# Kernel optimization log

Hardware: AMD Instinct MI355X
Metric: run time of the kernel (lower is better)

Reference implementation:

```python
import jax, jax.numpy as jnp
import numpy as np

HID = 768
POS = 768
TGT = 20
LBL = 30522
EPS = 1e-5


def layer_norm(x, g, b):
    mu = jnp.mean(x, axis=-1, keepdims=True)
    var = jnp.mean((x - mu) ** 2, axis=-1, keepdims=True)
    return (x - mu) * jax.lax.rsqrt(var + EPS) * g + b


def setup_inputs() -> dict:
    key = jax.random.key(0)
    ks = jax.random.split(key, 12)
    bs, n_node, num_pairs = 4, 512, 128
    inp = {
        "input_nodes": jax.random.normal(ks[0], (bs, n_node, HID), dtype=jnp.float32),
        "pairs": jax.random.randint(ks[1], (bs, num_pairs, 2), 0, n_node - 1, dtype=jnp.int64),
        "pos_emb": jax.random.normal(ks[2], (TGT, POS), dtype=jnp.float32) * 0.02,
        "W1": jax.random.normal(ks[3], (2 * HID + POS, HID), dtype=jnp.float32) * 0.02,
        "b1": jnp.zeros((HID,), dtype=jnp.float32),
        "g1": jnp.ones((HID,), dtype=jnp.float32),
        "be1": jnp.zeros((HID,), dtype=jnp.float32),
        "W2": jax.random.normal(ks[4], (HID, HID), dtype=jnp.float32) * 0.02,
        "b2": jnp.zeros((HID,), dtype=jnp.float32),
        "g2": jnp.ones((HID,), dtype=jnp.float32),
        "be2": jnp.zeros((HID,), dtype=jnp.float32),
        "Wd": jax.random.normal(ks[5], (HID, LBL), dtype=jnp.float32) * 0.02,
        "bd": jnp.zeros((LBL,), dtype=jnp.float32),
    }
    return inp


def reference(input_nodes, pairs, pos_emb, W1, b1, g1, be1, W2, b2, g2, be2, Wd, bd):
    bs, num_pairs, _ = pairs.shape
    dim = input_nodes.shape[-1]
    left = pairs[:, :, 0] + 1   # [bs, np]
    right = pairs[:, :, 1] + 1
    # gather paired node features: [bs, np, dim]
    lh = jnp.take_along_axis(input_nodes, left[:, :, None], axis=1)
    rh = jnp.take_along_axis(input_nodes, right[:, :, None], axis=1)
    R = bs * num_pairs
    lh = jnp.broadcast_to(lh.reshape(R, 1, dim), (R, TGT, dim))
    rh = jnp.broadcast_to(rh.reshape(R, 1, dim), (R, TGT, dim))
    pe = jnp.broadcast_to(pos_emb[None, :, :], (R, TGT, POS))
    x = jnp.concatenate((lh, rh, pe), axis=-1)  # [R, TGT, 2*HID+POS]
    h = layer_norm(jax.nn.gelu(x @ W1 + b1), g1, be1)
    h = layer_norm(jax.nn.gelu(h @ W2 + b2), g2, be2)
    return h @ Wd + bd  # [R, TGT, LBL]
```

## Files before the change

### kernel.cpp

```cpp
#include <hip/hip_runtime.h>
#include <stdint.h>
#include <math.h>

typedef unsigned short u16;
typedef unsigned int u32;

#define HID   768
#define TGT   20
#define LBL   30522
#define RPAIR 512
#define ROWS  10240
#define KCAT  1536
#define NPAD2 30720

typedef float  f32x4  __attribute__((ext_vector_type(4)));
typedef __bf16 bf16x8 __attribute__((ext_vector_type(8)));

__device__ __forceinline__ u16 f2bf(float f) {
  u32 u = __float_as_uint(f);
  u += 0x7fffu + ((u >> 16) & 1u);
  return (u16)(u >> 16);
}
__device__ __forceinline__ float bf2f(u16 h) {
  return __uint_as_float(((u32)h) << 16);
}
__device__ __forceinline__ float gelu_tanh(float x) {
  float x3 = x * x * x;
  float t = tanhf(0.7978845608028654f * (x + 0.044715f * x3));
  return 0.5f * x * (1.0f + t);
}

__device__ __forceinline__ void async16(u16* lds, const u16* g) {
  __builtin_amdgcn_global_load_lds(
      (__attribute__((address_space(1))) void*)const_cast<u16*>(g),
      (__attribute__((address_space(3))) void*)lds,
      16, 0, 0);
}

#define BARRIER() do { asm volatile("" ::: "memory"); __builtin_amdgcn_s_barrier(); asm volatile("" ::: "memory"); } while (0)

__global__ __launch_bounds__(256) void tconv_kernel(const float* __restrict__ B,
                                                    u16* __restrict__ Bt,
                                                    int K, int N, int Npad) {
  __shared__ u16 tile[32][34];
  int n0 = blockIdx.x * 32, k0 = blockIdx.y * 32;
  int tx = threadIdx.x & 31, ty = threadIdx.x >> 5;
#pragma unroll
  for (int i = 0; i < 4; i++) {
    int kk = ty + i * 8;
    int k = k0 + kk, n = n0 + tx;
    float v = (k < K && n < N) ? B[(size_t)k * N + n] : 0.0f;
    tile[kk][tx] = f2bf(v);
  }
  __syncthreads();
#pragma unroll
  for (int i = 0; i < 4; i++) {
    int nn = ty + i * 8;
    int n = n0 + nn, k = k0 + tx;
    if (n < Npad && k < K) Bt[(size_t)n * K + k] = tile[tx][nn];
  }
}

__global__ __launch_bounds__(256) void gather_kernel(const float* __restrict__ nodes,
                                                     const int* __restrict__ p32,
                                                     u16* __restrict__ A1) {
  int idx = blockIdx.x * 256 + threadIdx.x;
  if (idx >= RPAIR * KCAT) return;
  bool is64 = ((p32[1] | p32[3] | p32[5] | p32[7] | p32[9] | p32[11] | p32[13] | p32[15]) == 0);
  int r = idx / KCAT, c = idx - r * KCAT;
  int b = r >> 7, p = r & 127;
  int which = (c >= HID) ? 1 : 0;
  int cc = which ? (c - HID) : c;
  int slot = (b * 128 + p) * 2 + which;
  int node = (is64 ? p32[slot * 2] : p32[slot]) + 1;
  float v = nodes[((size_t)(b * 512 + node)) * HID + cc];
  A1[idx] = f2bf(v);
}

__global__ __launch_bounds__(256) void peproj_kernel(const float* __restrict__ pos_emb,
                                                     const float* __restrict__ W1,
                                                     const float* __restrict__ b1,
                                                     float* __restrict__ pep) {
  __shared__ float pe[HID];
  int t = blockIdx.x, tid = threadIdx.x;
  for (int i = tid; i < HID; i += 256) pe[i] = pos_emb[t * HID + i];
  __syncthreads();
  float acc0 = 0.f, acc1 = 0.f, acc2 = 0.f;
  const float* Wp = W1 + (size_t)KCAT * HID;
  for (int k = 0; k < HID; k++) {
    float p = pe[k];
    const float* wr = Wp + (size_t)k * HID;
    acc0 = fmaf(p, wr[tid], acc0);
    acc1 = fmaf(p, wr[tid + 256], acc1);
    acc2 = fmaf(p, wr[tid + 512], acc2);
  }
  pep[t * HID + tid]       = acc0 + b1[tid];
  pep[t * HID + tid + 256] = acc1 + b1[tid + 256];
  pep[t * HID + tid + 512] = acc2 + b1[tid + 512];
}

template <int EPI>
__global__ __launch_bounds__(256) void gemm_bt(const u16* __restrict__ A,
                                               const u16* __restrict__ Bt,
                                               const float* __restrict__ bias,
                                               float* __restrict__ Cf,
                                               u16* __restrict__ Cb,
                                               int N, int K) {
  __shared__ __align__(16) u16 As[128 * 32];
  __shared__ __align__(16) u16 Bs[128 * 32];
  const int tid  = threadIdx.x;
  const int lane = tid & 63;
  const int w    = tid >> 6;
  const int wr   = w >> 1, wc = w & 1;
  const int m0 = blockIdx.y * 128;
  const int n0 = blockIdx.x * 128;

  f32x4 acc[4][4];
  const f32x4 fzero = {0.f, 0.f, 0.f, 0.f};
#pragma unroll
  for (int m = 0; m < 4; m++)
#pragma unroll
    for (int n = 0; n < 4; n++) acc[m][n] = fzero;

  const int srow = lane >> 2;
  const int scol = (lane & 3) * 8;
  const int nkt = K >> 5;

  for (int kt = 0; kt < nkt; ++kt) {
    const int k0 = kt << 5;
#pragma unroll
    for (int j = 0; j < 2; j++) {
      int rbase = w * 32 + j * 16;
      async16(&As[rbase * 32], A + (size_t)(m0 + rbase + srow) * K + k0 + scol);
      async16(&Bs[rbase * 32], Bt + (size_t)(n0 + rbase + srow) * K + k0 + scol);
    }
    asm volatile("s_waitcnt vmcnt(0)" ::: "memory");
    __syncthreads();

    bf16x8 a[4], b[4];
    const int kk = (lane >> 4) * 8;
#pragma unroll
    for (int m = 0; m < 4; m++)
      a[m] = *reinterpret_cast<const bf16x8*>(&As[(wr * 64 + m * 16 + (lane & 15)) * 32 + kk]);
#pragma unroll
    for (int n = 0; n < 4; n++)
      b[n] = *reinterpret_cast<const bf16x8*>(&Bs[(wc * 64 + n * 16 + (lane & 15)) * 32 + kk]);
#pragma unroll
    for (int m = 0; m < 4; m++)
#pragma unroll
      for (int n = 0; n < 4; n++)
        acc[m][n] = __builtin_amdgcn_mfma_f32_16x16x32_bf16(a[m], b[n], acc[m][n], 0, 0, 0);
    __syncthreads();
  }

  const int rr = (lane >> 4) * 4;
  const int cc = lane & 15;
#pragma unroll
  for (int m = 0; m < 4; m++) {
#pragma unroll
    for (int n = 0; n < 4; n++) {
      int col = n0 + wc * 64 + n * 16 + cc;
#pragma unroll
      for (int j = 0; j < 4; j++) {
        int row = m0 + wr * 64 + m * 16 + rr + j;
        float v = acc[m][n][j];
        if (EPI == 0) {
          Cf[(size_t)row * N + col] = v;
        } else {
          v = gelu_tanh(v + bias[col]);
          Cb[(size_t)row * N + col] = f2bf(v);
        }
      }
    }
  }
}

__global__ __launch_bounds__(512, 2) void gemm256_head(const u16* __restrict__ A,
                                                       const u16* __restrict__ B,
                                                       const float* __restrict__ bias,
                                                       float* __restrict__ C) {
  __shared__ __align__(16) u16 As[2][256 * 64];
  __shared__ __align__(16) u16 Bs[2][256 * 64];
  const int tid  = threadIdx.x;
  const int lane = tid & 63;
  const int wid  = tid >> 6;
  const int wm   = wid >> 2;
  const int wn   = wid & 3;

  int orig = blockIdx.x;
  int l = (orig & 7) * 600 + (orig >> 3);
  int mt = l / 120, nt = l - mt * 120;
  const int m0 = mt * 256, n0 = nt * 256;
  const int nkt = 12;

  f32x4 acc[8][4];
  const f32x4 fzero = {0.f, 0.f, 0.f, 0.f};
#pragma unroll
  for (int mi = 0; mi < 8; mi++)
#pragma unroll
    for (int ni = 0; ni < 4; ni++) acc[mi][ni] = fzero;

  const int sl_r = lane >> 3;
  const int sl_c = ((lane & 7) ^ sl_r) * 8;
  auto stage_half = [&](const u16* src, int grow0, u16* ldsReg, int half, int ke0) {
#pragma unroll
    for (int j = 0; j < 2; j++) {
      int rowb = half * 128 + (j * 8 + wid) * 8;
      const u16* gp = src + (size_t)(grow0 + rowb + sl_r) * 768 + ke0 + sl_c;
      async16(ldsReg + rowb * 64, gp);
    }
  };
  auto lda = [&](const u16* buf, int mi, int ks) -> bf16x8 {
    int row = wm * 128 + mi * 16 + (lane & 15);
    int kch = ks * 4 + (lane >> 4);
    return *reinterpret_cast<const bf16x8*>(&buf[row * 64 + ((kch ^ (row & 7)) << 3)]);
  };
  auto ldb = [&](const u16* buf, int ni, int ks) -> bf16x8 {
    int row = wn * 64 + ni * 16 + (lane & 15);
    int kch = ks * 4 + (lane >> 4);
    return *reinterpret_cast<const bf16x8*>(&buf[row * 64 + ((kch ^ (row & 7)) << 3)]);
  };

  stage_half(A, m0, As[0], 0, 0);
  stage_half(A, m0, As[0], 1, 0);
  stage_half(B, n0, Bs[0], 0, 0);
  stage_half(B, n0, Bs[0], 1, 0);
  stage_half(A, m0, As[1], 0, 64);
  stage_half(A, m0, As[1], 1, 64);
  asm volatile("s_waitcnt vmcnt(4)" ::: "memory");
  __builtin_amdgcn_sched_barrier(0);
  __builtin_amdgcn_s_barrier();
  asm volatile("" ::: "memory");

  bf16x8 aF[8][2];
  bf16x8 bF[4][2];

#define MFMA_QUAD(MI0, NI0)                                                        \
  do {                                                                             \
    __builtin_amdgcn_s_setprio(1);                                                 \
    _Pragma("unroll") for (int mi = (MI0); mi < (MI0) + 4; ++mi)                   \
      _Pragma("unroll") for (int ni = (NI0); ni < (NI0) + 2; ++ni)                 \
        _Pragma("unroll") for (int ks = 0; ks < 2; ++ks)                           \
          acc[mi][ni] = __builtin_amdgcn_mfma_f32_16x16x32_bf16(aF[mi][ks], bF[ni][ks], acc[mi][ni], 0, 0, 0); \
    __builtin_amdgcn_s_setprio(0);                                                 \
  } while (0)

#define WAIT_LGKM() do { asm volatile("s_waitcnt lgkmcnt(0)" ::: "memory"); __builtin_amdgcn_sched_barrier(0); } while (0)

  for (int t = 0; t < nkt; ++t) {
    const u16* Ab = As[t & 1];
    const u16* Bb = Bs[t & 1];
    u16* Bnext = Bs[(t + 1) & 1];
    u16* Acur  = As[t & 1];
    const int ke1 = (t + 1) * 64, ke2 = (t + 2) * 64;
    const bool sB = (t + 1) < nkt, sA = (t + 2) < nkt;

#pragma unroll
    for (int mi = 0; mi < 4; ++mi)
#pragma unroll
      for (int ks = 0; ks < 2; ++ks) aF[mi][ks] = lda(Ab, mi, ks);
#pragma unroll
    for (int ni = 0; ni < 2; ++ni)
#pragma unroll
      for (int ks = 0; ks < 2; ++ks) bF[ni][ks] = ldb(Bb, ni, ks);
    if (sB) stage_half(B, n0, Bnext, 0, ke1);
    BARRIER();
    WAIT_LGKM();
    MFMA_QUAD(0, 0);
    BARRIER();

#pragma unroll
    for (int mi = 4; mi < 8; ++mi)
#pragma unroll
      for (int ks = 0; ks < 2; ++ks) aF[mi][ks] = lda(Ab, mi, ks);
    if (sB) stage_half(B, n0, Bnext, 1, ke1);
    BARRIER();
    WAIT_LGKM();
    MFMA_QUAD(4, 0);
    BARRIER();

#pragma unroll
    for (int ni = 2; ni < 4; ++ni)
#pragma unroll
      for (int ks = 0; ks < 2; ++ks) bF[ni][ks] = ldb(Bb, ni, ks);
    if (sA) stage_half(A, m0, Acur, 0, ke2);
    BARRIER();
    WAIT_LGKM();
    MFMA_QUAD(4, 2);
    BARRIER();

    if (sA) stage_half(A, m0, Acur, 1, ke2);
    BARRIER();
    MFMA_QUAD(0, 2);
    if (t + 2 < nkt) {
      asm volatile("s_waitcnt vmcnt(4)" ::: "memory");
    } else if (t + 1 < nkt) {
      asm volatile("s_waitcnt vmcnt(0)" ::: "memory");
    }
    __builtin_amdgcn_sched_barrier(0);
    BARRIER();
  }
#undef MFMA_QUAD
#undef WAIT_LGKM

  const int r0 = m0 + wm * 128;
  const int c0 = n0 + wn * 64;
  const int rr = (lane >> 4) * 4;
  const int ccl = lane & 15;
#pragma unroll
  for (int ni = 0; ni < 4; ++ni) {
    int col = c0 + ni * 16 + ccl;
    if (col < LBL) {
      float bv = bias[col];
#pragma unroll
      for (int mi = 0; mi < 8; ++mi)
#pragma unroll
        for (int j = 0; j < 4; ++j) {
          int row = r0 + mi * 16 + rr + j;
          C[(size_t)row * LBL + col] = acc[mi][ni][j] + bv;
        }
    }
  }
}

__global__ __launch_bounds__(256) void fuse1_kernel(const float* __restrict__ s,
                                                    const float* __restrict__ pep,
                                                    const float* __restrict__ g1,
                                                    const float* __restrict__ be1,
                                                    u16* __restrict__ h1) {
  __shared__ float red[8];
  int g = blockIdx.x, tid = threadIdx.x;
  int r = g / TGT, t = g - r * TGT;
  const float* sr = s + (size_t)r * HID;
  const float* pt = pep + (size_t)t * HID;
  float y[3], s1 = 0.f, s2 = 0.f;
#pragma unroll
  for (int i = 0; i < 3; i++) {
    int j = tid + i * 256;
    float x = sr[j] + pt[j];
    y[i] = gelu_tanh(x);
    s1 += y[i];
    s2 += y[i] * y[i];
  }
#pragma unroll
  for (int off = 32; off > 0; off >>= 1) {
    s1 += __shfl_down(s1, off);
    s2 += __shfl_down(s2, off);
  }
  if ((tid & 63) == 0) { red[tid >> 6] = s1; red[4 + (tid >> 6)] = s2; }
  __syncthreads();
  float mean = (red[0] + red[1] + red[2] + red[3]) * (1.0f / HID);
  float var  = (red[4] + red[5] + red[6] + red[7]) * (1.0f / HID) - mean * mean;
  float inv  = rsqrtf(var + 1e-5f);
#pragma unroll
  for (int i = 0; i < 3; i++) {
    int j = tid + i * 256;
    h1[(size_t)g * HID + j] = f2bf((y[i] - mean) * inv * g1[j] + be1[j]);
  }
}

__global__ __launch_bounds__(256) void fuse2_kernel(const u16* __restrict__ G,
                                                    const float* __restrict__ g2,
                                                    const float* __restrict__ be2,
                                                    u16* __restrict__ h2) {
  __shared__ float red[8];
  int g = blockIdx.x, tid = threadIdx.x;
  const u16* gr = G + (size_t)g * HID;
  float y[3], s1 = 0.f, s2 = 0.f;
#pragma unroll
  for (int i = 0; i < 3; i++) {
    int j = tid + i * 256;
    y[i] = bf2f(gr[j]);
    s1 += y[i];
    s2 += y[i] * y[i];
  }
#pragma unroll
  for (int off = 32; off > 0; off >>= 1) {
    s1 += __shfl_down(s1, off);
    s2 += __shfl_down(s2, off);
  }
  if ((tid & 63) == 0) { red[tid >> 6] = s1; red[4 + (tid >> 6)] = s2; }
  __syncthreads();
  float mean = (red[0] + red[1] + red[2] + red[3]) * (1.0f / HID);
  float var  = (red[4] + red[5] + red[6] + red[7]) * (1.0f / HID) - mean * mean;
  float inv  = rsqrtf(var + 1e-5f);
#pragma unroll
  for (int i = 0; i < 3; i++) {
    int j = tid + i * 256;
    h2[(size_t)g * HID + j] = f2bf((y[i] - mean) * inv * g2[j] + be2[j]);
  }
}

extern "C" void kernel_launch(void* const* d_in, const int* in_sizes, int n_in,
                              void* d_out, int out_size, void* d_ws, size_t ws_size,
                              hipStream_t stream) {
  const float* input_nodes = (const float*)d_in[0];
  const int*   pairs       = (const int*)d_in[1];
  const float* pos_emb     = (const float*)d_in[2];
  const float* W1  = (const float*)d_in[3];
  const float* b1  = (const float*)d_in[4];
  const float* g1  = (const float*)d_in[5];
  const float* be1 = (const float*)d_in[6];
  const float* W2  = (const float*)d_in[7];
  const float* b2  = (const float*)d_in[8];
  const float* g2  = (const float*)d_in[9];
  const float* be2 = (const float*)d_in[10];
  const float* Wd  = (const float*)d_in[11];
  const float* bd  = (const float*)d_in[12];
  float* out = (float*)d_out;

  char* ws = (char*)d_ws;
  u16*   WdT   = (u16*)(ws + 0);
  u16*   W2T   = (u16*)(ws + 47185920);
  u16*   W1lrT = (u16*)(ws + 48365568);
  u16*   A1    = (u16*)(ws + 50724864);
  float* pep   = (float*)(ws + 52297728);
  float* sbuf  = (float*)(ws + 52359168);
  u16*   h1    = (u16*)(ws + 53932032);
  u16*   G     = (u16*)(ws + 69660672);

  tconv_kernel<<<dim3(960, 24), 256, 0, stream>>>(Wd, WdT, HID, LBL, NPAD2);
  tconv_kernel<<<dim3(24, 24), 256, 0, stream>>>(W2, W2T, HID, HID, HID);
  tconv_kernel<<<dim3(24, 48), 256, 0, stream>>>(W1, W1lrT, KCAT, HID, HID);
  gather_kernel<<<dim3((RPAIR * KCAT + 255) / 256), 256, 0, stream>>>(input_nodes, pairs, A1);
  peproj_kernel<<<dim3(TGT), 256, 0, stream>>>(pos_emb, W1, b1, pep);

  gemm_bt<0><<<dim3(6, 4), 256, 0, stream>>>(A1, W1lrT, nullptr, sbuf, nullptr, HID, KCAT);
  fuse1_kernel<<<dim3(ROWS), 256, 0, stream>>>(sbuf, pep, g1, be1, h1);

  gemm_bt<1><<<dim3(6, 80), 256, 0, stream>>>(h1, W2T, b2, nullptr, G, HID, HID);
  fuse2_kernel<<<dim3(ROWS), 256, 0, stream>>>(G, g2, be2, G);

  gemm256_head<<<dim3(4800), 512, 0, stream>>>(G, WdT, bd, out);
}
```

Measured before the change: 1.296 ms.

## Make head GEMM persistent, streaming tiles continuously across k-loop boundaries

```diff
diff --git a/kernel.cpp b/kernel.cpp
--- a/kernel.cpp
+++ b/kernel.cpp
@@ -38,6 +38,8 @@
 }
 
 #define BARRIER() do { asm volatile("" ::: "memory"); __builtin_amdgcn_s_barrier(); asm volatile("" ::: "memory"); } while (0)
+#define VMWAIT8() do { asm volatile("s_waitcnt vmcnt(8)" ::: "memory"); __builtin_amdgcn_sched_barrier(0); } while (0)
+#define VMWAIT0() do { asm volatile("s_waitcnt vmcnt(0)" ::: "memory"); __builtin_amdgcn_sched_barrier(0); } while (0)
 
 __global__ __launch_bounds__(256) void tconv_kernel(const float* __restrict__ B,
                                                     u16* __restrict__ Bt,
@@ -175,10 +177,10 @@
   }
 }
 
-__global__ __launch_bounds__(512, 2) void gemm256_head(const u16* __restrict__ A,
-                                                       const u16* __restrict__ B,
-                                                       const float* __restrict__ bias,
-                                                       float* __restrict__ C) {
+__global__ __launch_bounds__(512, 2) void gemm256_stream(const u16* __restrict__ A,
+                                                         const u16* __restrict__ B,
+                                                         const float* __restrict__ bias,
+                                                         float* __restrict__ C) {
   __shared__ __align__(16) u16 As[2][256 * 64];
   __shared__ __align__(16) u16 Bs[2][256 * 64];
   const int tid  = threadIdx.x;
@@ -187,11 +189,11 @@
   const int wm   = wid >> 2;
   const int wn   = wid & 3;
 
-  int orig = blockIdx.x;
-  int l = (orig & 7) * 600 + (orig >> 3);
-  int mt = l / 120, nt = l - mt * 120;
-  const int m0 = mt * 256, n0 = nt * 256;
-  const int nkt = 12;
+  const int x  = blockIdx.x & 7;
+  const int jb = blockIdx.x >> 3;
+  const int t0 = (600 * jb) >> 5;
+  const int t1 = (600 * (jb + 1)) >> 5;
+  const int Q  = (t1 - t0) * 12;
 
   f32x4 acc[8][4];
   const f32x4 fzero = {0.f, 0.f, 0.f, 0.f};
@@ -202,12 +204,22 @@
 
   const int sl_r = lane >> 3;
   const int sl_c = ((lane & 7) ^ sl_r) * 8;
-  auto stage_half = [&](const u16* src, int grow0, u16* ldsReg, int half, int ke0) {
-#pragma unroll
-    for (int j = 0; j < 2; j++) {
-      int rowb = half * 128 + (j * 8 + wid) * 8;
-      const u16* gp = src + (size_t)(grow0 + rowb + sl_r) * 768 + ke0 + sl_c;
-      async16(ldsReg + rowb * 64, gp);
+
+  auto stage = [&](int q) {
+    int tt = t0 + q / 12;
+    int kt = q - (q / 12) * 12;
+    int mt = 5 * x + tt / 120;
+    int nt = tt - (tt / 120) * 120;
+    const int k0 = kt * 64;
+    u16* Ab = As[q & 1];
+    u16* Bb = Bs[q & 1];
+    const u16* Ag = A + (size_t)(mt * 256) * 768 + k0;
+    const u16* Bg = B + (size_t)(nt * 256) * 768 + k0;
+#pragma unroll
+    for (int jj = 0; jj < 4; jj++) {
+      int rbase = wid * 32 + jj * 8;
+      async16(Ab + rbase * 64, Ag + (size_t)(rbase + sl_r) * 768 + sl_c);
+      async16(Bb + rbase * 64, Bg + (size_t)(rbase + sl_r) * 768 + sl_c);
     }
   };
   auto lda = [&](const u16* buf, int mi, int ks) -> bf16x8 {
@@ -221,105 +233,58 @@
     return *reinterpret_cast<const bf16x8*>(&buf[row * 64 + ((kch ^ (row & 7)) << 3)]);
   };
 
-  stage_half(A, m0, As[0], 0, 0);
-  stage_half(A, m0, As[0], 1, 0);
-  stage_half(B, n0, Bs[0], 0, 0);
-  stage_half(B, n0, Bs[0], 1, 0);
-  stage_half(A, m0, As[1], 0, 64);
-  stage_half(A, m0, As[1], 1, 64);
-  asm volatile("s_waitcnt vmcnt(4)" ::: "memory");
-  __builtin_amdgcn_sched_barrier(0);
-  __builtin_amdgcn_s_barrier();
-  asm volatile("" ::: "memory");
-
-  bf16x8 aF[8][2];
-  bf16x8 bF[4][2];
-
-#define MFMA_QUAD(MI0, NI0)                                                        \
-  do {                                                                             \
-    __builtin_amdgcn_s_setprio(1);                                                 \
-    _Pragma("unroll") for (int mi = (MI0); mi < (MI0) + 4; ++mi)                   \
-      _Pragma("unroll") for (int ni = (NI0); ni < (NI0) + 2; ++ni)                 \
-        _Pragma("unroll") for (int ks = 0; ks < 2; ++ks)                           \
-          acc[mi][ni] = __builtin_amdgcn_mfma_f32_16x16x32_bf16(aF[mi][ks], bF[ni][ks], acc[mi][ni], 0, 0, 0); \
-    __builtin_amdgcn_s_setprio(0);                                                 \
-  } while (0)
-
-#define WAIT_LGKM() do { asm volatile("s_waitcnt lgkmcnt(0)" ::: "memory"); __builtin_amdgcn_sched_barrier(0); } while (0)
-
-  for (int t = 0; t < nkt; ++t) {
-    const u16* Ab = As[t & 1];
-    const u16* Bb = Bs[t & 1];
-    u16* Bnext = Bs[(t + 1) & 1];
-    u16* Acur  = As[t & 1];
-    const int ke1 = (t + 1) * 64, ke2 = (t + 2) * 64;
-    const bool sB = (t + 1) < nkt, sA = (t + 2) < nkt;
-
-#pragma unroll
-    for (int mi = 0; mi < 4; ++mi)
-#pragma unroll
-      for (int ks = 0; ks < 2; ++ks) aF[mi][ks] = lda(Ab, mi, ks);
-#pragma unroll
-    for (int ni = 0; ni < 2; ++ni)
-#pragma unroll
-      for (int ks = 0; ks < 2; ++ks) bF[ni][ks] = ldb(Bb, ni, ks);
-    if (sB) stage_half(B, n0, Bnext, 0, ke1);
+  const int rr  = (lane >> 4) * 4;
+  const int ccl = lane & 15;
+
+  stage(0);
+  for (int q = 0; q < Q; ++q) {
+    if (q + 1 < Q) { stage(q + 1); VMWAIT8(); }
+    else          { VMWAIT0(); }
     BARRIER();
-    WAIT_LGKM();
-    MFMA_QUAD(0, 0);
+
+    const u16* Ab = As[q & 1];
+    const u16* Bb = Bs[q & 1];
+#pragma unroll
+    for (int ks = 0; ks < 2; ++ks) {
+      bf16x8 aF[8], bF[4];
+#pragma unroll
+      for (int mi = 0; mi < 8; ++mi) aF[mi] = lda(Ab, mi, ks);
+#pragma unroll
+      for (int ni = 0; ni < 4; ++ni) bF[ni] = ldb(Bb, ni, ks);
+      __builtin_amdgcn_s_setprio(1);
+#pragma unroll
+      for (int mi = 0; mi < 8; ++mi)
+#pragma unroll
+        for (int ni = 0; ni < 4; ++ni)
+          acc[mi][ni] = __builtin_amdgcn_mfma_f32_16x16x32_bf16(aF[mi], bF[ni], acc[mi][ni], 0, 0, 0);
+      __builtin_amdgcn_s_setprio(0);
+    }
+
+    int kt = q - (q / 12) * 12;
+    if (kt == 11) {
+      int tt = t0 + q / 12;
+      int mt = 5 * x + tt / 120;
+      int nt = tt - (tt / 120) * 120;
+      int r0 = mt * 256 + wm * 128;
+      int c0 = nt * 256 + wn * 64;
+#pragma unroll
+      for (int ni = 0; ni < 4; ++ni) {
+        int col = c0 + ni * 16 + ccl;
+        if (col < LBL) {
+          float bv = bias[col];
+#pragma unroll
+          for (int mi = 0; mi < 8; ++mi)
+#pragma unroll
+            for (int j = 0; j < 4; ++j)
+              C[(size_t)(r0 + mi * 16 + rr + j) * LBL + col] = acc[mi][ni][j] + bv;
+        }
+      }
+#pragma unroll
+      for (int mi = 0; mi < 8; mi++)
+#pragma unroll
+        for (int ni = 0; ni < 4; ni++) acc[mi][ni] = fzero;
+    }
     BARRIER();
-
-#pragma unroll
-    for (int mi = 4; mi < 8; ++mi)
-#pragma unroll
-      for (int ks = 0; ks < 2; ++ks) aF[mi][ks] = lda(Ab, mi, ks);
-    if (sB) stage_half(B, n0, Bnext, 1, ke1);
-    BARRIER();
-    WAIT_LGKM();
-    MFMA_QUAD(4, 0);
-    BARRIER();
-
-#pragma unroll
-    for (int ni = 2; ni < 4; ++ni)
-#pragma unroll
-      for (int ks = 0; ks < 2; ++ks) bF[ni][ks] = ldb(Bb, ni, ks);
-    if (sA) stage_half(A, m0, Acur, 0, ke2);
-    BARRIER();
-    WAIT_LGKM();
-    MFMA_QUAD(4, 2);
-    BARRIER();
-
-    if (sA) stage_half(A, m0, Acur, 1, ke2);
-    BARRIER();
-    MFMA_QUAD(0, 2);
-    if (t + 2 < nkt) {
-      asm volatile("s_waitcnt vmcnt(4)" ::: "memory");
-    } else if (t + 1 < nkt) {
-      asm volatile("s_waitcnt vmcnt(0)" ::: "memory");
-    }
-    __builtin_amdgcn_sched_barrier(0);
-    BARRIER();
-  }
-#undef MFMA_QUAD
-#undef WAIT_LGKM
-
-  const int r0 = m0 + wm * 128;
-  const int c0 = n0 + wn * 64;
-  const int rr = (lane >> 4) * 4;
-  const int ccl = lane & 15;
-#pragma unroll
-  for (int ni = 0; ni < 4; ++ni) {
-    int col = c0 + ni * 16 + ccl;
-    if (col < LBL) {
-      float bv = bias[col];
-#pragma unroll
-      for (int mi = 0; mi < 8; ++mi)
-#pragma unroll
-        for (int j = 0; j < 4; ++j) {
-          int row = r0 + mi * 16 + rr + j;
-          C[(size_t)row * LBL + col] = acc[mi][ni][j] + bv;
-        }
-    }
   }
 }
 
@@ -431,5 +396,5 @@
   gemm_bt<1><<<dim3(6, 80), 256, 0, stream>>>(h1, W2T, b2, nullptr, G, HID, HID);
   fuse2_kernel<<<dim3(ROWS), 256, 0, stream>>>(G, g2, be2, G);
 
-  gemm256_head<<<dim3(4800), 512, 0, stream>>>(G, WdT, bd, out);
-}
+  gemm256_stream<<<dim3(256), 512, 0, stream>>>(G, WdT, bd, out);
+}
```

After: 1.181 ms. 1.1x faster.
